# Kernel tuning notes

Measured on AMD Instinct MI355X. Metric: run time of the kernel, lower is better.

The kernel has to match this reference:

```python
import jax, jax.numpy as jnp
import numpy as np

ALPHA = 0.2  # LeakyReLU negative slope
NEG_INF = -9e15


def setup_inputs() -> dict:
    key = jax.random.key(0)
    k1, k2, k3, k4 = jax.random.split(key, 4)
    B, T, N, F_in, F_out = 8, 8, 1024, 64, 64
    h = jax.random.normal(k1, (B, T, N, F_in), dtype=jnp.float32)
    adj = jax.random.randint(k2, (B, T, N, N), 0, 2, dtype=jnp.int32)
    # xavier_uniform with gain=1.414
    def xavier(k, shape, gain=1.414):
        fan_in, fan_out = shape[0], shape[1]
        bound = gain * np.sqrt(6.0 / (fan_in + fan_out))
        return jax.random.uniform(k, shape, jnp.float32, -bound, bound)
    W = xavier(k3, (F_in, F_out))
    a = xavier(k4, (2 * F_out, 1))
    return {"h": h, "adj": adj, "W": W, "a": a}


def reference(h, adj, W, a):
    # h: [B,T,N,F_in], adj: [B,T,N,N], W: [F_in,F_out], a: [2*F_out,1]
    F_out = W.shape[1]
    Wh = h @ W  # [B,T,N,F_out]
    a1 = a[:F_out, 0]   # source half
    a2 = a[F_out:, 0]   # target half
    s1 = Wh @ a1        # [B,T,N]
    s2 = Wh @ a2        # [B,T,N]
    # e[...,i,j] = LeakyReLU(s1_i + s2_j)  == original concat-linear score
    e = jax.nn.leaky_relu(s1[..., :, None] + s2[..., None, :], negative_slope=ALPHA)
    att = jnp.where(adj > 0, e, NEG_INF)
    att = jax.nn.softmax(att, axis=-1)  # [B,T,N,N]
    # dropout omitted: reference runs in eval mode (p only active in training)
    h_prime = att @ Wh  # [B,T,N,F_out]
    return jax.nn.elu(h_prime)  # concat=True path
```

## Files before the change

### kernel.cpp

```cpp
#include <hip/hip_runtime.h>

#define NN 1024
#define FF 64
#define NBT 64

typedef float f32x4 __attribute__((ext_vector_type(4)));
typedef short s16x8 __attribute__((ext_vector_type(8)));

__device__ __forceinline__ short f2bf(float f) {
    unsigned u = __builtin_bit_cast(unsigned, f);
    u = (u + 0x7FFFu + ((u >> 16) & 1u)) >> 16;
    return (short)u;
}

__global__ __launch_bounds__(256) void k1(const float* __restrict__ h,
                                          const float* __restrict__ W,
                                          const float* __restrict__ a,
                                          short* __restrict__ WhT,
                                          float* __restrict__ s1g,
                                          float* __restrict__ s2g) {
    __shared__ float Wl[64 * 64];
    __shared__ float al[128];
    __shared__ float s1sh[128], s2sh[128];
    const int blk = blockIdx.x;
    const int bt = blk >> 3;
    const int rbase = (blk & 7) * 128;
    const int t = threadIdx.x;

    for (int i = t; i < 1024; i += 256)
        ((f32x4*)Wl)[i] = ((const f32x4*)W)[i];
    if (t < 32) ((f32x4*)al)[t] = ((const f32x4*)a)[t];
    __syncthreads();

    const int row = rbase + (t & 127);
    const int half = t >> 7;
    const float* hrow = h + ((size_t)bt * NN + row) * FF;
    float hv[64];
#pragma unroll
    for (int i = 0; i < 16; i++)
        ((f32x4*)hv)[i] = ((const f32x4*)hrow)[i];

    float s1 = 0.f, s2 = 0.f;
    short* wt = WhT + (size_t)bt * FF * NN + row;
#pragma unroll
    for (int cgi = 0; cgi < 8; cgi++) {
        const int cg = half * 8 + cgi;
        f32x4 acc = {0.f, 0.f, 0.f, 0.f};
#pragma unroll
        for (int k = 0; k < 64; k++) {
            f32x4 w4 = ((const f32x4*)Wl)[k * 16 + cg];
            acc += hv[k] * w4;
        }
        const int c0 = cg * 4;
        s1 += acc.x * al[c0] + acc.y * al[c0 + 1] + acc.z * al[c0 + 2] + acc.w * al[c0 + 3];
        s2 += acc.x * al[64 + c0] + acc.y * al[64 + c0 + 1] + acc.z * al[64 + c0 + 2] + acc.w * al[64 + c0 + 3];
        wt[(size_t)(c0 + 0) * NN] = f2bf(acc.x);
        wt[(size_t)(c0 + 1) * NN] = f2bf(acc.y);
        wt[(size_t)(c0 + 2) * NN] = f2bf(acc.z);
        wt[(size_t)(c0 + 3) * NN] = f2bf(acc.w);
    }
    if (half == 1) { s1sh[t & 127] = s1; s2sh[t & 127] = s2; }
    __syncthreads();
    if (half == 0) {
        s1g[bt * NN + row] = s1 + s1sh[t];
        s2g[bt * NN + row] = s2 + s2sh[t];
    }
}

__global__ __launch_bounds__(256) void k2(const int* __restrict__ adj,
                                          const short* __restrict__ WhT,
                                          const float* __restrict__ s1g,
                                          const float* __restrict__ s2g,
                                          float* __restrict__ out) {
    __shared__ float s2l[NN];

    const int bx = blockIdx.x;
    const int bt = bx >> 4;
    const int ibase = (bx & 15) * 64;
    const int t = threadIdx.x;
    const int wv = t >> 6;
    const int l = t & 63;
    const int m = l & 15;
    const int q = l >> 4;

    ((f32x4*)s2l)[t] = ((const f32x4*)(s2g + (size_t)bt * NN))[t];

    const int row = ibase + wv * 16 + m;
    const float s1v = s1g[bt * NN + row];

    const int* adjp = adj + ((size_t)bt * NN + row) * NN + q * 8;
    const short* whp = WhT + (size_t)bt * FF * NN + (size_t)m * NN + q * 8;

    f32x4 acc0 = {0.f, 0.f, 0.f, 0.f};
    f32x4 acc1 = {0.f, 0.f, 0.f, 0.f};
    f32x4 acc2 = {0.f, 0.f, 0.f, 0.f};
    f32x4 acc3 = {0.f, 0.f, 0.f, 0.f};
    float rs = 0.f;

    int4 ca0 = *(const int4*)(adjp);
    int4 ca1 = *(const int4*)(adjp + 4);
    s16x8 cb0 = *(const s16x8*)(whp);
    s16x8 cb1 = *(const s16x8*)(whp + 16 * NN);
    s16x8 cb2 = *(const s16x8*)(whp + 32 * NN);
    s16x8 cb3 = *(const s16x8*)(whp + 48 * NN);

    __syncthreads();

    for (int jt = 0; jt < 32; jt++) {
        const int jn = (jt < 31) ? (jt + 1) * 32 : 31 * 32;
        int4 na0 = *(const int4*)(adjp + jn);
        int4 na1 = *(const int4*)(adjp + jn + 4);
        s16x8 nb0 = *(const s16x8*)(whp + jn);
        s16x8 nb1 = *(const s16x8*)(whp + 16 * NN + jn);
        s16x8 nb2 = *(const s16x8*)(whp + 32 * NN + jn);
        s16x8 nb3 = *(const s16x8*)(whp + 48 * NN + jn);

        f32x4 s2a = *(const f32x4*)&s2l[jt * 32 + q * 8];
        f32x4 s2b = *(const f32x4*)&s2l[jt * 32 + q * 8 + 4];
        int aj[8] = {ca0.x, ca0.y, ca0.z, ca0.w, ca1.x, ca1.y, ca1.z, ca1.w};
        float sv[8] = {s2a.x, s2a.y, s2a.z, s2a.w, s2b.x, s2b.y, s2b.z, s2b.w};
        s16x8 af;
#pragma unroll
        for (int u = 0; u < 8; u++) {
            float e = s1v + sv[u];
            e = fmaxf(e, 0.2f * e);
            e = fminf(e, 60.f);
            float p = (aj[u] > 0) ? __expf(e) : 0.f;
            rs += p;
            af[u] = f2bf(p);
        }

        acc0 = __builtin_amdgcn_mfma_f32_16x16x32_bf16(af, cb0, acc0, 0, 0, 0);
        acc1 = __builtin_amdgcn_mfma_f32_16x16x32_bf16(af, cb1, acc1, 0, 0, 0);
        acc2 = __builtin_amdgcn_mfma_f32_16x16x32_bf16(af, cb2, acc2, 0, 0, 0);
        acc3 = __builtin_amdgcn_mfma_f32_16x16x32_bf16(af, cb3, acc3, 0, 0, 0);

        ca0 = na0; ca1 = na1;
        cb0 = nb0; cb1 = nb1; cb2 = nb2; cb3 = nb3;
    }

    rs += __shfl_xor(rs, 16);
    rs += __shfl_xor(rs, 32);

    float rinv[4];
#pragma unroll
    for (int e = 0; e < 4; e++) {
        float rv = __shfl(rs, q * 4 + e);
        rinv[e] = rv > 0.f ? 1.f / rv : 0.f;
    }
    float* outp = out + ((size_t)bt * NN + ibase + wv * 16 + q * 4) * FF + m;
#pragma unroll
    for (int e = 0; e < 4; e++) {
        float v0 = acc0[e] * rinv[e];
        float v1 = acc1[e] * rinv[e];
        float v2 = acc2[e] * rinv[e];
        float v3 = acc3[e] * rinv[e];
        v0 = v0 > 0.f ? v0 : expm1f(v0);
        v1 = v1 > 0.f ? v1 : expm1f(v1);
        v2 = v2 > 0.f ? v2 : expm1f(v2);
        v3 = v3 > 0.f ? v3 : expm1f(v3);
        float* o = outp + (size_t)e * FF;
        o[0]  = v0;
        o[16] = v1;
        o[32] = v2;
        o[48] = v3;
    }
}

extern "C" void kernel_launch(void* const* d_in, const int* in_sizes, int n_in,
                              void* d_out, int out_size, void* d_ws, size_t ws_size,
                              hipStream_t stream) {
    const float* h  = (const float*)d_in[0];
    const int*  adj = (const int*)d_in[1];
    const float* W  = (const float*)d_in[2];
    const float* a  = (const float*)d_in[3];
    float* out = (float*)d_out;

    short* WhT = (short*)d_ws;
    float* s1  = (float*)((char*)d_ws + (size_t)NBT * FF * NN * 2);
    float* s2  = s1 + NBT * NN;

    k1<<<512, 256, 0, stream>>>(h, W, a, WhT, s1, s2);
    k2<<<1024, 256, 0, stream>>>(adj, WhT, s1, s2, out);
}
```

Before: 421.0 us.

## Double-buffer attention loads, use exp2, packed bf16 convert, MFMA row sums

Scores are pre-scaled by 1/ln2 in k1 so k2 can call exp2f directly, and the manual bf16 rounding is replaced with the packed v_cvt_pk_bf16_f32 instruction. The k2 loop now keeps two sets of prefetched adj/WhT tiles in flight instead of one, and launch bounds request higher occupancy. Row sums come from an extra MFMA against a ones vector instead of scalar adds plus shuffles, so the normaliser now uses bf16-rounded probabilities. The deeper prefetch raises register pressure, which may conflict with the occupancy hint.

```diff
diff --git a/kernel.cpp b/kernel.cpp
--- a/kernel.cpp
+++ b/kernel.cpp
@@ -3,9 +3,11 @@
 #define NN 1024
 #define FF 64
 #define NBT 64
+#define INV_LN2 1.44269504088896f
 
 typedef float f32x4 __attribute__((ext_vector_type(4)));
 typedef short s16x8 __attribute__((ext_vector_type(8)));
+typedef unsigned u32x4 __attribute__((ext_vector_type(4)));
 
 __device__ __forceinline__ short f2bf(float f) {
     unsigned u = __builtin_bit_cast(unsigned, f);
@@ -62,16 +64,16 @@
     if (half == 1) { s1sh[t & 127] = s1; s2sh[t & 127] = s2; }
     __syncthreads();
     if (half == 0) {
-        s1g[bt * NN + row] = s1 + s1sh[t];
-        s2g[bt * NN + row] = s2 + s2sh[t];
-    }
-}
-
-__global__ __launch_bounds__(256) void k2(const int* __restrict__ adj,
-                                          const short* __restrict__ WhT,
-                                          const float* __restrict__ s1g,
-                                          const float* __restrict__ s2g,
-                                          float* __restrict__ out) {
+        s1g[bt * NN + row] = (s1 + s1sh[t]) * INV_LN2;
+        s2g[bt * NN + row] = (s2 + s2sh[t]) * INV_LN2;
+    }
+}
+
+__global__ __launch_bounds__(256, 4) void k2(const int* __restrict__ adj,
+                                             const short* __restrict__ WhT,
+                                             const float* __restrict__ s1g,
+                                             const float* __restrict__ s2g,
+                                             float* __restrict__ out) {
     __shared__ float s2l[NN];
 
     const int bx = blockIdx.x;
@@ -95,59 +97,78 @@
     f32x4 acc1 = {0.f, 0.f, 0.f, 0.f};
     f32x4 acc2 = {0.f, 0.f, 0.f, 0.f};
     f32x4 acc3 = {0.f, 0.f, 0.f, 0.f};
-    float rs = 0.f;
-
-    int4 ca0 = *(const int4*)(adjp);
-    int4 ca1 = *(const int4*)(adjp + 4);
-    s16x8 cb0 = *(const s16x8*)(whp);
-    s16x8 cb1 = *(const s16x8*)(whp + 16 * NN);
-    s16x8 cb2 = *(const s16x8*)(whp + 32 * NN);
-    s16x8 cb3 = *(const s16x8*)(whp + 48 * NN);
-
-    __syncthreads();
-
-    for (int jt = 0; jt < 32; jt++) {
-        const int jn = (jt < 31) ? (jt + 1) * 32 : 31 * 32;
-        int4 na0 = *(const int4*)(adjp + jn);
-        int4 na1 = *(const int4*)(adjp + jn + 4);
-        s16x8 nb0 = *(const s16x8*)(whp + jn);
-        s16x8 nb1 = *(const s16x8*)(whp + 16 * NN + jn);
-        s16x8 nb2 = *(const s16x8*)(whp + 32 * NN + jn);
-        s16x8 nb3 = *(const s16x8*)(whp + 48 * NN + jn);
-
+    f32x4 accR = {0.f, 0.f, 0.f, 0.f};
+    const s16x8 ones = {0x3F80, 0x3F80, 0x3F80, 0x3F80, 0x3F80, 0x3F80, 0x3F80, 0x3F80};
+
+#define LDT(J, A0, A1, B0, B1, B2, B3) do {            \
+        const int _o = ((J) < 32 ? (J) : 31) * 32;     \
+        A0 = *(const int4*)(adjp + _o);                \
+        A1 = *(const int4*)(adjp + _o + 4);            \
+        B0 = *(const s16x8*)(whp + _o);                \
+        B1 = *(const s16x8*)(whp + 16 * NN + _o);      \
+        B2 = *(const s16x8*)(whp + 32 * NN + _o);      \
+        B3 = *(const s16x8*)(whp + 48 * NN + _o);      \
+    } while (0)
+
+    auto compute = [&](int jt, int4 ca0, int4 ca1,
+                       s16x8 cb0, s16x8 cb1, s16x8 cb2, s16x8 cb3) {
         f32x4 s2a = *(const f32x4*)&s2l[jt * 32 + q * 8];
         f32x4 s2b = *(const f32x4*)&s2l[jt * 32 + q * 8 + 4];
-        int aj[8] = {ca0.x, ca0.y, ca0.z, ca0.w, ca1.x, ca1.y, ca1.z, ca1.w};
-        float sv[8] = {s2a.x, s2a.y, s2a.z, s2a.w, s2b.x, s2b.y, s2b.z, s2b.w};
-        s16x8 af;
+        const int aj[8] = {ca0.x, ca0.y, ca0.z, ca0.w, ca1.x, ca1.y, ca1.z, ca1.w};
+        const float sv[8] = {s2a.x, s2a.y, s2a.z, s2a.w, s2b.x, s2b.y, s2b.z, s2b.w};
+        float p[8];
 #pragma unroll
         for (int u = 0; u < 8; u++) {
             float e = s1v + sv[u];
             e = fmaxf(e, 0.2f * e);
-            e = fminf(e, 60.f);
-            float p = (aj[u] > 0) ? __expf(e) : 0.f;
-            rs += p;
-            af[u] = f2bf(p);
-        }
+            e = fminf(e, 86.0f);
+            float pe = exp2f(e);
+            p[u] = (aj[u] > 0) ? pe : 0.f;
+        }
+        unsigned w0, w1, w2, w3;
+        asm("v_cvt_pk_bf16_f32 %0, %1, %2" : "=v"(w0) : "v"(p[0]), "v"(p[1]));
+        asm("v_cvt_pk_bf16_f32 %0, %1, %2" : "=v"(w1) : "v"(p[2]), "v"(p[3]));
+        asm("v_cvt_pk_bf16_f32 %0, %1, %2" : "=v"(w2) : "v"(p[4]), "v"(p[5]));
+        asm("v_cvt_pk_bf16_f32 %0, %1, %2" : "=v"(w3) : "v"(p[6]), "v"(p[7]));
+        u32x4 wq = {w0, w1, w2, w3};
+        s16x8 af = __builtin_bit_cast(s16x8, wq);
 
         acc0 = __builtin_amdgcn_mfma_f32_16x16x32_bf16(af, cb0, acc0, 0, 0, 0);
         acc1 = __builtin_amdgcn_mfma_f32_16x16x32_bf16(af, cb1, acc1, 0, 0, 0);
         acc2 = __builtin_amdgcn_mfma_f32_16x16x32_bf16(af, cb2, acc2, 0, 0, 0);
         acc3 = __builtin_amdgcn_mfma_f32_16x16x32_bf16(af, cb3, acc3, 0, 0, 0);
-
-        ca0 = na0; ca1 = na1;
-        cb0 = nb0; cb1 = nb1; cb2 = nb2; cb3 = nb3;
-    }
-
-    rs += __shfl_xor(rs, 16);
-    rs += __shfl_xor(rs, 32);
+        accR = __builtin_amdgcn_mfma_f32_16x16x32_bf16(af, ones, accR, 0, 0, 0);
+    };
+
+    int4 a0A, a1A; s16x8 b0A, b1A, b2A, b3A;
+    int4 a0B, a1B; s16x8 b0B, b1B, b2B, b3B;
+
+    __syncthreads();
+
+    LDT(0, a0A, a1A, b0A, b1A, b2A, b3A);
+    LDT(1, a0B, a1B, b0B, b1B, b2B, b3B);
+
+    for (int jt = 0; jt < 32; jt += 2) {
+        {
+            int4 ta0 = a0A, ta1 = a1A;
+            s16x8 t0 = b0A, t1 = b1A, t2 = b2A, t3 = b3A;
+            LDT(jt + 2, a0A, a1A, b0A, b1A, b2A, b3A);
+            compute(jt, ta0, ta1, t0, t1, t2, t3);
+        }
+        {
+            int4 ta0 = a0B, ta1 = a1B;
+            s16x8 t0 = b0B, t1 = b1B, t2 = b2B, t3 = b3B;
+            LDT(jt + 3, a0B, a1B, b0B, b1B, b2B, b3B);
+            compute(jt + 1, ta0, ta1, t0, t1, t2, t3);
+        }
+    }
+#undef LDT
 
     float rinv[4];
 #pragma unroll
-    for (int e = 0; e < 4; e++) {
-        float rv = __shfl(rs, q * 4 + e);
-        rinv[e] = rv > 0.f ? 1.f / rv : 0.f;
-    }
+    for (int e = 0; e < 4; e++)
+        rinv[e] = accR[e] > 0.f ? 1.f / accR[e] : 0.f;
+
     float* outp = out + ((size_t)bt * NN + ibase + wv * 16 + q * 4) * FF + m;
 #pragma unroll
     for (int e = 0; e < 4; e++) {
```

After: 461.2 us. +9.5%, slower.

## Split attention key range across wave pairs, MFMA row sums, exp2 scores

Applied to the files above, without the earlier changes.

The attention kernel now gives each block 32 rows and splits the key dimension between two waves per 16-row tile. The halves are combined through shared memory before normalisation and ELU, doubling the grid. Row sums are computed by an extra MFMA against a ones vector instead of a scalar accumulation and shuffles. Scores are prescaled by 1/ln2 in the first kernel so exp2 can replace exp, and occupancy is hinted with launch bounds. These add a shared-memory exchange, a block barrier and one more MFMA per step. Half the waves sit idle during the epilogue.

```diff
diff --git a/kernel.cpp b/kernel.cpp
--- a/kernel.cpp
+++ b/kernel.cpp
@@ -3,6 +3,7 @@
 #define NN 1024
 #define FF 64
 #define NBT 64
+#define INV_LN2 1.44269504088896f
 
 typedef float f32x4 __attribute__((ext_vector_type(4)));
 typedef short s16x8 __attribute__((ext_vector_type(8)));
@@ -62,32 +63,37 @@
     if (half == 1) { s1sh[t & 127] = s1; s2sh[t & 127] = s2; }
     __syncthreads();
     if (half == 0) {
-        s1g[bt * NN + row] = s1 + s1sh[t];
-        s2g[bt * NN + row] = s2 + s2sh[t];
+        s1g[bt * NN + row] = (s1 + s1sh[t]) * INV_LN2;
+        s2g[bt * NN + row] = (s2 + s2sh[t]) * INV_LN2;
     }
 }
 
-__global__ __launch_bounds__(256) void k2(const int* __restrict__ adj,
-                                          const short* __restrict__ WhT,
-                                          const float* __restrict__ s1g,
-                                          const float* __restrict__ s2g,
-                                          float* __restrict__ out) {
+__global__ __launch_bounds__(256, 8) void k2(const int* __restrict__ adj,
+                                             const short* __restrict__ WhT,
+                                             const float* __restrict__ s1g,
+                                             const float* __restrict__ s2g,
+                                             float* __restrict__ out) {
     __shared__ float s2l[NN];
+    __shared__ __align__(16) float xch[2][64][24];
 
     const int bx = blockIdx.x;
-    const int bt = bx >> 4;
-    const int ibase = (bx & 15) * 64;
+    const int bt = bx >> 5;
+    const int rbase = (bx & 31) * 32;
     const int t = threadIdx.x;
     const int wv = t >> 6;
+    const int pr = wv >> 1;
+    const int jh = wv & 1;
     const int l = t & 63;
     const int m = l & 15;
     const int q = l >> 4;
 
     ((f32x4*)s2l)[t] = ((const f32x4*)(s2g + (size_t)bt * NN))[t];
 
-    const int row = ibase + wv * 16 + m;
+    const int row = rbase + pr * 16 + m;
     const float s1v = s1g[bt * NN + row];
 
+    const int jt0 = jh * 16;
+    const int jtN = jt0 + 15;
     const int* adjp = adj + ((size_t)bt * NN + row) * NN + q * 8;
     const short* whp = WhT + (size_t)bt * FF * NN + (size_t)m * NN + q * 8;
 
@@ -95,19 +101,20 @@
     f32x4 acc1 = {0.f, 0.f, 0.f, 0.f};
     f32x4 acc2 = {0.f, 0.f, 0.f, 0.f};
     f32x4 acc3 = {0.f, 0.f, 0.f, 0.f};
-    float rs = 0.f;
+    f32x4 accR = {0.f, 0.f, 0.f, 0.f};
+    const s16x8 ones = {0x3F80, 0x3F80, 0x3F80, 0x3F80, 0x3F80, 0x3F80, 0x3F80, 0x3F80};
 
-    int4 ca0 = *(const int4*)(adjp);
-    int4 ca1 = *(const int4*)(adjp + 4);
-    s16x8 cb0 = *(const s16x8*)(whp);
-    s16x8 cb1 = *(const s16x8*)(whp + 16 * NN);
-    s16x8 cb2 = *(const s16x8*)(whp + 32 * NN);
-    s16x8 cb3 = *(const s16x8*)(whp + 48 * NN);
+    int4 ca0 = *(const int4*)(adjp + jt0 * 32);
+    int4 ca1 = *(const int4*)(adjp + jt0 * 32 + 4);
+    s16x8 cb0 = *(const s16x8*)(whp + jt0 * 32);
+    s16x8 cb1 = *(const s16x8*)(whp + 16 * NN + jt0 * 32);
+    s16x8 cb2 = *(const s16x8*)(whp + 32 * NN + jt0 * 32);
+    s16x8 cb3 = *(const s16x8*)(whp + 48 * NN + jt0 * 32);
 
     __syncthreads();
 
-    for (int jt = 0; jt < 32; jt++) {
-        const int jn = (jt < 31) ? (jt + 1) * 32 : 31 * 32;
+    for (int jt = jt0; jt <= jtN; jt++) {
+        const int jn = (jt < jtN ? jt + 1 : jtN) * 32;
         int4 na0 = *(const int4*)(adjp + jn);
         int4 na1 = *(const int4*)(adjp + jn + 4);
         s16x8 nb0 = *(const s16x8*)(whp + jn);
@@ -117,16 +124,16 @@
 
         f32x4 s2a = *(const f32x4*)&s2l[jt * 32 + q * 8];
         f32x4 s2b = *(const f32x4*)&s2l[jt * 32 + q * 8 + 4];
-        int aj[8] = {ca0.x, ca0.y, ca0.z, ca0.w, ca1.x, ca1.y, ca1.z, ca1.w};
-        float sv[8] = {s2a.x, s2a.y, s2a.z, s2a.w, s2b.x, s2b.y, s2b.z, s2b.w};
+        const int aj[8] = {ca0.x, ca0.y, ca0.z, ca0.w, ca1.x, ca1.y, ca1.z, ca1.w};
+        const float sv[8] = {s2a.x, s2a.y, s2a.z, s2a.w, s2b.x, s2b.y, s2b.z, s2b.w};
         s16x8 af;
 #pragma unroll
         for (int u = 0; u < 8; u++) {
             float e = s1v + sv[u];
             e = fmaxf(e, 0.2f * e);
-            e = fminf(e, 60.f);
-            float p = (aj[u] > 0) ? __expf(e) : 0.f;
-            rs += p;
+            e = fminf(e, 86.0f);
+            float pe = exp2f(e);
+            float p = (aj[u] > 0) ? pe : 0.f;
             af[u] = f2bf(p);
         }
 
@@ -134,36 +141,43 @@
         acc1 = __builtin_amdgcn_mfma_f32_16x16x32_bf16(af, cb1, acc1, 0, 0, 0);
         acc2 = __builtin_amdgcn_mfma_f32_16x16x32_bf16(af, cb2, acc2, 0, 0, 0);
         acc3 = __builtin_amdgcn_mfma_f32_16x16x32_bf16(af, cb3, acc3, 0, 0, 0);
+        accR = __builtin_amdgcn_mfma_f32_16x16x32_bf16(af, ones, accR, 0, 0, 0);
 
         ca0 = na0; ca1 = na1;
         cb0 = nb0; cb1 = nb1; cb2 = nb2; cb3 = nb3;
     }
 
-    rs += __shfl_xor(rs, 16);
-    rs += __shfl_xor(rs, 32);
+    if (jh == 1) {
+        f32x4* x = (f32x4*)&xch[pr][l][0];
+        x[0] = acc0; x[1] = acc1; x[2] = acc2; x[3] = acc3; x[4] = accR;
+    }
+    __syncthreads();
+    if (jh == 0) {
+        const f32x4* x = (const f32x4*)&xch[pr][l][0];
+        acc0 += x[0]; acc1 += x[1]; acc2 += x[2]; acc3 += x[3]; accR += x[4];
 
-    float rinv[4];
+        float rinv[4];
 #pragma unroll
-    for (int e = 0; e < 4; e++) {
-        float rv = __shfl(rs, q * 4 + e);
-        rinv[e] = rv > 0.f ? 1.f / rv : 0.f;
-    }
-    float* outp = out + ((size_t)bt * NN + ibase + wv * 16 + q * 4) * FF + m;
+        for (int e = 0; e < 4; e++)
+            rinv[e] = accR[e] > 0.f ? 1.f / accR[e] : 0.f;
+
+        float* outp = out + ((size_t)bt * NN + rbase + pr * 16 + q * 4) * FF + m;
 #pragma unroll
-    for (int e = 0; e < 4; e++) {
-        float v0 = acc0[e] * rinv[e];
-        float v1 = acc1[e] * rinv[e];
-        float v2 = acc2[e] * rinv[e];
-        float v3 = acc3[e] * rinv[e];
-        v0 = v0 > 0.f ? v0 : expm1f(v0);
-        v1 = v1 > 0.f ? v1 : expm1f(v1);
-        v2 = v2 > 0.f ? v2 : expm1f(v2);
-        v3 = v3 > 0.f ? v3 : expm1f(v3);
-        float* o = outp + (size_t)e * FF;
-        o[0]  = v0;
-        o[16] = v1;
-        o[32] = v2;
-        o[48] = v3;
+        for (int e = 0; e < 4; e++) {
+            float v0 = acc0[e] * rinv[e];
+            float v1 = acc1[e] * rinv[e];
+            float v2 = acc2[e] * rinv[e];
+            float v3 = acc3[e] * rinv[e];
+            v0 = v0 > 0.f ? v0 : expm1f(v0);
+            v1 = v1 > 0.f ? v1 : expm1f(v1);
+            v2 = v2 > 0.f ? v2 : expm1f(v2);
+            v3 = v3 > 0.f ? v3 : expm1f(v3);
+            float* o = outp + (size_t)e * FF;
+            o[0]  = v0;
+            o[16] = v1;
+            o[32] = v2;
+            o[48] = v3;
+        }
     }
 }
 
@@ -181,5 +195,5 @@
     float* s2  = s1 + NBT * NN;
 
     k1<<<512, 256, 0, stream>>>(h, W, a, WhT, s1, s2);
-    k2<<<1024, 256, 0, stream>>>(adj, WhT, s1, s2, out);
+    k2<<<2048, 256, 0, stream>>>(adj, WhT, s1, s2, out);
 }
```

Result: slower. 458.3 us (+8.9%).

## Factor exp of LeakyReLU into per-node exponentials and bit-pack adjacency

Applied to the files above, without the earlier changes.

The score exponential is split into products of per-node exponentials: exp(max(x,0.2x)) = max(e^s1*e^s2, e^{0.2 s1}*e^{0.2 s2}). This removes the per-element exp from the inner loop. The adjacency block is prefetched with coalesced loads and packed into bitmasks in shared memory using ballots, and the row sum is computed by an extra MFMA against a ones vector instead of scalar adds and shuffles. It also drops the max-clamp in favour of 1e9 caps, which could lose precision or overflow bf16 range for large scores. The denominator now sums the bf16-rounded values, so it matches the numerator's rounding.

```diff
diff --git a/kernel.cpp b/kernel.cpp
--- a/kernel.cpp
+++ b/kernel.cpp
@@ -3,6 +3,7 @@
 #define NN 1024
 #define FF 64
 #define NBT 64
+#define INV_LN2 1.44269504088896f
 
 typedef float f32x4 __attribute__((ext_vector_type(4)));
 typedef short s16x8 __attribute__((ext_vector_type(8)));
@@ -62,17 +63,18 @@
     if (half == 1) { s1sh[t & 127] = s1; s2sh[t & 127] = s2; }
     __syncthreads();
     if (half == 0) {
-        s1g[bt * NN + row] = s1 + s1sh[t];
-        s2g[bt * NN + row] = s2 + s2sh[t];
-    }
-}
-
-__global__ __launch_bounds__(256) void k2(const int* __restrict__ adj,
-                                          const short* __restrict__ WhT,
-                                          const float* __restrict__ s1g,
-                                          const float* __restrict__ s2g,
-                                          float* __restrict__ out) {
-    __shared__ float s2l[NN];
+        s1g[bt * NN + row] = (s1 + s1sh[t]) * INV_LN2;
+        s2g[bt * NN + row] = (s2 + s2sh[t]) * INV_LN2;
+    }
+}
+
+__global__ __launch_bounds__(256, 4) void k2(const int* __restrict__ adj,
+                                             const short* __restrict__ WhT,
+                                             const float* __restrict__ s1g,
+                                             const float* __restrict__ s2g,
+                                             float* __restrict__ out) {
+    __shared__ float F1[NN], F2[NN];
+    __shared__ __align__(8) unsigned adjb[64 * 34];
 
     const int bx = blockIdx.x;
     const int bt = bx >> 4;
@@ -83,22 +85,45 @@
     const int m = l & 15;
     const int q = l >> 4;
 
-    ((f32x4*)s2l)[t] = ((const f32x4*)(s2g + (size_t)bt * NN))[t];
+    for (int i = t; i < NN; i += 256) {
+        float s2v = s2g[bt * NN + i];
+        F1[i] = fminf(exp2f(s2v), 1e9f);
+        F2[i] = fminf(exp2f(0.2f * s2v), 1e9f);
+    }
+
+    {
+        const int* ap = adj + ((size_t)bt * NN + ibase + wv * 16) * NN + l;
+        for (int g = 0; g < 16; g++) {
+            int v[16];
+#pragma unroll
+            for (int r = 0; r < 16; r++)
+                v[r] = ap[(size_t)r * NN + g * 64];
+            unsigned long long keep = 0;
+#pragma unroll
+            for (int r = 0; r < 16; r++) {
+                unsigned long long bal = __ballot(v[r] != 0);
+                if (l == r) keep = bal;
+            }
+            if (l < 16)
+                *(unsigned long long*)&adjb[(wv * 16 + l) * 34 + g * 2] = keep;
+        }
+    }
 
     const int row = ibase + wv * 16 + m;
     const float s1v = s1g[bt * NN + row];
-
-    const int* adjp = adj + ((size_t)bt * NN + row) * NN + q * 8;
+    const float E1 = fminf(exp2f(s1v), 1e9f);
+    const float E2 = fminf(exp2f(0.2f * s1v), 1e9f);
+
     const short* whp = WhT + (size_t)bt * FF * NN + (size_t)m * NN + q * 8;
+    const unsigned* myrow = &adjb[(wv * 16 + m) * 34];
 
     f32x4 acc0 = {0.f, 0.f, 0.f, 0.f};
     f32x4 acc1 = {0.f, 0.f, 0.f, 0.f};
     f32x4 acc2 = {0.f, 0.f, 0.f, 0.f};
     f32x4 acc3 = {0.f, 0.f, 0.f, 0.f};
-    float rs = 0.f;
-
-    int4 ca0 = *(const int4*)(adjp);
-    int4 ca1 = *(const int4*)(adjp + 4);
+    f32x4 accR = {0.f, 0.f, 0.f, 0.f};
+    const s16x8 ones = {0x3F80, 0x3F80, 0x3F80, 0x3F80, 0x3F80, 0x3F80, 0x3F80, 0x3F80};
+
     s16x8 cb0 = *(const s16x8*)(whp);
     s16x8 cb1 = *(const s16x8*)(whp + 16 * NN);
     s16x8 cb2 = *(const s16x8*)(whp + 32 * NN);
@@ -107,26 +132,27 @@
     __syncthreads();
 
     for (int jt = 0; jt < 32; jt++) {
-        const int jn = (jt < 31) ? (jt + 1) * 32 : 31 * 32;
-        int4 na0 = *(const int4*)(adjp + jn);
-        int4 na1 = *(const int4*)(adjp + jn + 4);
+        const int jn = (jt < 31 ? jt + 1 : 31) * 32;
         s16x8 nb0 = *(const s16x8*)(whp + jn);
         s16x8 nb1 = *(const s16x8*)(whp + 16 * NN + jn);
         s16x8 nb2 = *(const s16x8*)(whp + 32 * NN + jn);
         s16x8 nb3 = *(const s16x8*)(whp + 48 * NN + jn);
 
-        f32x4 s2a = *(const f32x4*)&s2l[jt * 32 + q * 8];
-        f32x4 s2b = *(const f32x4*)&s2l[jt * 32 + q * 8 + 4];
-        int aj[8] = {ca0.x, ca0.y, ca0.z, ca0.w, ca1.x, ca1.y, ca1.z, ca1.w};
-        float sv[8] = {s2a.x, s2a.y, s2a.z, s2a.w, s2b.x, s2b.y, s2b.z, s2b.w};
+        const unsigned word = myrow[jt];
+        const unsigned mb = (word >> (q * 8)) & 255u;
+
+        f32x4 f1a = *(const f32x4*)&F1[jt * 32 + q * 8];
+        f32x4 f1b = *(const f32x4*)&F1[jt * 32 + q * 8 + 4];
+        f32x4 f2a = *(const f32x4*)&F2[jt * 32 + q * 8];
+        f32x4 f2b = *(const f32x4*)&F2[jt * 32 + q * 8 + 4];
+        const float v1[8] = {f1a.x, f1a.y, f1a.z, f1a.w, f1b.x, f1b.y, f1b.z, f1b.w};
+        const float v2[8] = {f2a.x, f2a.y, f2a.z, f2a.w, f2b.x, f2b.y, f2b.z, f2b.w};
+
         s16x8 af;
 #pragma unroll
         for (int u = 0; u < 8; u++) {
-            float e = s1v + sv[u];
-            e = fmaxf(e, 0.2f * e);
-            e = fminf(e, 60.f);
-            float p = (aj[u] > 0) ? __expf(e) : 0.f;
-            rs += p;
+            float pe = fmaxf(E1 * v1[u], E2 * v2[u]);
+            float p = (mb & (1u << u)) ? pe : 0.f;
             af[u] = f2bf(p);
         }
 
@@ -134,36 +160,32 @@
         acc1 = __builtin_amdgcn_mfma_f32_16x16x32_bf16(af, cb1, acc1, 0, 0, 0);
         acc2 = __builtin_amdgcn_mfma_f32_16x16x32_bf16(af, cb2, acc2, 0, 0, 0);
         acc3 = __builtin_amdgcn_mfma_f32_16x16x32_bf16(af, cb3, acc3, 0, 0, 0);
-
-        ca0 = na0; ca1 = na1;
+        accR = __builtin_amdgcn_mfma_f32_16x16x32_bf16(af, ones, accR, 0, 0, 0);
+
         cb0 = nb0; cb1 = nb1; cb2 = nb2; cb3 = nb3;
     }
 
-    rs += __shfl_xor(rs, 16);
-    rs += __shfl_xor(rs, 32);
-
     float rinv[4];
 #pragma unroll
-    for (int e = 0; e < 4; e++) {
-        float rv = __shfl(rs, q * 4 + e);
-        rinv[e] = rv > 0.f ? 1.f / rv : 0.f;
-    }
+    for (int e = 0; e < 4; e++)
+        rinv[e] = accR[e] > 0.f ? 1.f / accR[e] : 0.f;
+
     float* outp = out + ((size_t)bt * NN + ibase + wv * 16 + q * 4) * FF + m;
 #pragma unroll
     for (int e = 0; e < 4; e++) {
         float v0 = acc0[e] * rinv[e];
-        float v1 = acc1[e] * rinv[e];
-        float v2 = acc2[e] * rinv[e];
-        float v3 = acc3[e] * rinv[e];
-        v0 = v0 > 0.f ? v0 : expm1f(v0);
-        v1 = v1 > 0.f ? v1 : expm1f(v1);
-        v2 = v2 > 0.f ? v2 : expm1f(v2);
-        v3 = v3 > 0.f ? v3 : expm1f(v3);
+        float v1o = acc1[e] * rinv[e];
+        float v2o = acc2[e] * rinv[e];
+        float v3o = acc3[e] * rinv[e];
+        v0  = v0  > 0.f ? v0  : expm1f(v0);
+        v1o = v1o > 0.f ? v1o : expm1f(v1o);
+        v2o = v2o > 0.f ? v2o : expm1f(v2o);
+        v3o = v3o > 0.f ? v3o : expm1f(v3o);
         float* o = outp + (size_t)e * FF;
         o[0]  = v0;
-        o[16] = v1;
-        o[32] = v2;
-        o[48] = v3;
+        o[16] = v1o;
+        o[32] = v2o;
+        o[48] = v3o;
     }
 }
 
```

Measured after the change: 463.6 us. 1.1x slower.
